# Optimization experiments

Measured on AMD Instinct MI355X. Metric: run time of the kernel, lower is better.

## Reference

```python
import jax, jax.numpy as jnp
import numpy as np

ALPHA = 0.5
EPS = 1e-6


def setup_inputs() -> dict:
    key = jax.random.key(0)
    k1, k2, k3 = jax.random.split(key, 3)
    B, N = 8192, 4096
    y_pred = jax.random.uniform(k1, (B, N), dtype=jnp.float32)
    y_true = jax.random.randint(k2, (B, N), 0, 2).astype(jnp.float32)
    depth_weights = jax.random.uniform(k3, (B, N), dtype=jnp.float32)
    return {"y_pred": y_pred, "y_true": y_true, "depth_weights": depth_weights}


def reference(y_pred, y_true, depth_weights):
    B, N = y_true.shape
    # --- weighted BCE ---
    bce = -(y_true * jnp.log(y_pred + EPS) + (1.0 - y_true) * jnp.log(1.0 - y_pred + EPS))
    wbce = jnp.mean(depth_weights * bce)

    # --- continuity-weighted loss: max run of correct predictions per row ---
    y_bin = (y_pred > 0.5).astype(y_true.dtype)
    correct = (y_bin == y_true)  # bool [B, N]
    idx = jnp.arange(N, dtype=jnp.int32)
    # position (1-based) of most recent incorrect element; 0 if none yet
    reset = jnp.where(correct, 0, idx + 1)  # [B, N]
    last_reset = jax.lax.cummax(reset, axis=1)  # [B, N]
    streak = (idx + 1)[None, :] - last_reset  # current run length at each position
    max_streak = jnp.max(streak, axis=1).astype(jnp.float32)  # [B]
    cwl = jnp.mean(1.0 - max_streak / N)

    return ALPHA * wbce + (1.0 - ALPHA) * cwl
```

## Files before the change

kernel.cpp:

```cpp
#include <hip/hip_runtime.h>

#define EPS 1e-6f
#define LN2F 0.69314718055994530942f


#define ONE(pc, tc, wc, bit) {                                   \
    const bool  tb  = (tc) != 0.0f;   \
    const float sel = tb ? (pc) : 1.0f - (pc);                   \
    sum = fmaf((wc), __log2f(sel + EPS), sum);                   \
    nibs |= (unsigned)(((pc) > 0.5f) == tb) << (bit); }

#define CHUNK(P, T, W, q) {                  \
    ONE(P.x, T.x, W.x, 8*(q)+0)              \
    ONE(P.y, T.y, W.y, 8*(q)+1)              \
    ONE(P.z, T.z, W.z, 8*(q)+2)              \
    ONE(P.w, T.w, W.w, 8*(q)+3) }

__global__ __launch_bounds__(256, 4) void phaseA_kernel(
        const float* __restrict__ yp, const float* __restrict__ yt,
        const float* __restrict__ dw,
        unsigned short* __restrict__ masks,
        float* __restrict__ wv_wbce,
        long tiles_total) {
    const int lane = threadIdx.x & 63;
    const int wave = threadIdx.x >> 6;
    const long wgid = (long)blockIdx.x * 4 + wave;
    const long nwv  = (long)gridDim.x * 4;

    __shared__ unsigned nibbuf[256];

    float sum = 0.0f;

    for (long t = wgid; t < tiles_total; t += nwv) {
        const long base = t * 1024 + lane * 4;
        const float4* pp = (const float4*)(yp + base);
        const float4* tp = (const float4*)(yt + base);
        const float4* wp = (const float4*)(dw + base);

        const float4 p0 = pp[0],   p1 = pp[64],  p2 = pp[128], p3 = pp[192];
        const float4 t0 = tp[0],   t1 = tp[64],  t2 = tp[128], t3 = tp[192];
        const float4 w0 = wp[0],   w1 = wp[64],  w2 = wp[128], w3 = wp[192];

        unsigned nibs = 0;
        CHUNK(p0, t0, w0, 0)
        CHUNK(p1, t1, w1, 1)
        CHUNK(p2, t2, w2, 2)
        CHUNK(p3, t3, w3, 3)

        nibbuf[wave * 64 + lane] = nibs;
        asm volatile("s_waitcnt lgkmcnt(0)" ::: "memory");
        const uint4 d = *(const uint4*)&nibbuf[wave * 64 + 4 * (lane & 15)];
        const int qs = (lane >> 4) * 8;
        const unsigned mask = ((d.x >> qs) & 0xFu)
                            | (((d.y >> qs) & 0xFu) << 4)
                            | (((d.z >> qs) & 0xFu) << 8)
                            | (((d.w >> qs) & 0xFu) << 12);
        masks[t * 64 + (lane >> 4) * 16 + (lane & 15)] = (unsigned short)mask;
    }

    #pragma unroll
    for (int off = 32; off; off >>= 1) sum += __shfl_down(sum, off);
    if (lane == 0) wv_wbce[wgid] = sum;
}

__global__ __launch_bounds__(256, 4) void phaseB_kernel(
        const unsigned short* __restrict__ masks,
        int* __restrict__ wv_streak, long rows) {
    const int lane = threadIdx.x & 63;
    const int wave = threadIdx.x >> 6;
    const long wgid = (long)blockIdx.x * 4 + wave;
    const long nwv  = (long)gridDim.x * 4;

    int acc = 0;
    for (long r = wgid; r < rows; r += nwv) {
        const unsigned long long m =
            *(const unsigned long long*)(masks + r * 256 + lane * 4);
        int pre, suf, mx;
        if (~m == 0ULL) {
            pre = suf = mx = 64;
        } else {
            pre = __builtin_ctzll(~m);
            suf = __builtin_clzll(~m);
            const unsigned long long pp1 = m;
            const unsigned long long pp2 = pp1 & (pp1 << 1);
            const unsigned long long pp4 = pp2 & (pp2 << 2);
            const unsigned long long pp8 = pp4 & (pp4 << 4);
            const unsigned long long pp16 = pp8 & (pp8 << 8);
            const unsigned long long pp32 = pp16 & (pp16 << 16);
            unsigned long long z; int len;
            if (pp32)      { z = pp32; len = 32; }
            else if (pp16) { z = pp16; len = 16; }
            else if (pp8)  { z = pp8;  len = 8; }
            else if (pp4)  { z = pp4;  len = 4; }
            else if (pp2)  { z = pp2;  len = 2; }
            else           { z = pp1;  len = 1; }
            { const unsigned long long q = (z << 16) & pp16; if (q) { z = q; len += 16; } }
            { const unsigned long long q = (z << 8)  & pp8;  if (q) { z = q; len += 8; } }
            { const unsigned long long q = (z << 4)  & pp4;  if (q) { z = q; len += 4; } }
            { const unsigned long long q = (z << 2)  & pp2;  if (q) { z = q; len += 2; } }
            { const unsigned long long q = (z << 1)  & pp1;  if (q) { z = q; len += 1; } }
            mx = m ? len : 0;
        }

        int alen = 64;
        #pragma unroll
        for (int off = 1; off < 64; off <<= 1) {
            const int bpre = __shfl_down(pre, off);
            const int bsuf = __shfl_down(suf, off);
            const int bmx  = __shfl_down(mx,  off);
            const int npre = (pre == alen) ? (alen + bpre) : pre;
            const int nsuf = (bsuf == alen) ? (alen + suf) : bsuf;
            mx  = max(max(mx, bmx), suf + bpre);
            pre = npre; suf = nsuf; alen <<= 1;
        }
        if (lane == 0) acc += mx;
    }
    if (lane == 0) wv_streak[wgid] = acc;
}

__global__ __launch_bounds__(1024) void finalize_kernel(
        const float* __restrict__ wv_wbce, int nA,
        const int* __restrict__ wv_streak, int nB,
        long long total_elems, float* __restrict__ out) {
    double s = 0.0;
    long long st = 0;
    for (int i = threadIdx.x; i < nA; i += 1024) s  += (double)wv_wbce[i];
    for (int i = threadIdx.x; i < nB; i += 1024) st += (long long)wv_streak[i];
    __shared__ double sd[1024];
    __shared__ long long sl[1024];
    sd[threadIdx.x] = s; sl[threadIdx.x] = st;
    __syncthreads();
    for (int o = 512; o; o >>= 1) {
        if (threadIdx.x < o) {
            sd[threadIdx.x] += sd[threadIdx.x + o];
            sl[threadIdx.x] += sl[threadIdx.x + o];
        }
        __syncthreads();
    }
    if (threadIdx.x == 0) {
        const double total = (double)total_elems;
        const double wbce = -LN2F * sd[0] / total;
        const double cwl  = 1.0 - (double)sl[0] / total;
        out[0] = (float)(0.5 * wbce + 0.5 * cwl);
    }
}

struct RunStats { int len, pre, suf, mx; };
__device__ inline RunStats rcombine(const RunStats& a, const RunStats& b) {
    RunStats r;
    r.len = a.len + b.len;
    r.pre = (a.pre == a.len) ? (a.len + b.pre) : a.pre;
    r.suf = (b.suf == b.len) ? (b.len + a.suf) : b.suf;
    r.mx  = max(max(a.mx, b.mx), a.suf + b.pre);
    return r;
}

__global__ __launch_bounds__(256) void fb_row_kernel(
        const float* __restrict__ yp, const float* __restrict__ yt,
        const float* __restrict__ dw,
        float* __restrict__ row_wbce, int* __restrict__ row_streak) {
    const int row  = blockIdx.x;
    const int lane = threadIdx.x & 63;
    const int wave = threadIdx.x >> 6;
    const long base = (long)row * 4096 + wave * 1024 + lane * 4;
    const float4* pp = (const float4*)(yp + base);
    const float4* tp = (const float4*)(yt + base);
    const float4* wp = (const float4*)(dw + base);

    float sum = 0.0f;
    unsigned nibs = 0;
    #pragma unroll
    for (int q = 0; q < 4; ++q) {
        const float4 P = pp[q * 64];
        const float4 T = tp[q * 64];
        const float4 W = wp[q * 64];
        CHUNK(P, T, W, q)
    }
    __shared__ unsigned nibbuf[256];
    nibbuf[wave * 64 + lane] = nibs;
    __syncthreads();
    const uint4 d = *(const uint4*)&nibbuf[wave * 64 + 4 * (lane & 15)];
    const int qs = (lane >> 4) * 8;
    const unsigned mask = ((d.x >> qs) & 0xFu) | (((d.y >> qs) & 0xFu) << 4)
                        | (((d.z >> qs) & 0xFu) << 8) | (((d.w >> qs) & 0xFu) << 12);
    const int pre = __builtin_ctz(~mask);
    const int suf = __builtin_clz(~(mask << 16));
    int mx;
    {
        const unsigned p1 = mask, p2 = p1 & (p1 << 1), p4 = p2 & (p2 << 2), p8 = p4 & (p4 << 4);
        unsigned z; int len;
        if (p8) { z = p8; len = 8; } else if (p4) { z = p4; len = 4; }
        else if (p2) { z = p2; len = 2; } else { z = p1; len = 1; }
        { const unsigned q2 = (z << 8) & p8; if (q2) { z = q2; len += 8; } }
        { const unsigned q2 = (z << 4) & p4; if (q2) { z = q2; len += 4; } }
        { const unsigned q2 = (z << 2) & p2; if (q2) { z = q2; len += 2; } }
        { const unsigned q2 = (z << 1) & p1; if (q2) { z = q2; len += 1; } }
        mx = mask ? len : 0;
    }
    #pragma unroll
    for (int off = 32; off; off >>= 1) sum += __shfl_down(sum, off);
    int packed = pre | (suf << 10) | (mx << 20);
    int alen = 16;
    #pragma unroll
    for (int off = 1; off < 32; off <<= 1) {
        const int o = __shfl_down(packed, off);
        const int apre = packed & 1023, asuf = (packed >> 10) & 1023, amx = packed >> 20;
        const int bpre = o & 1023, bsuf = (o >> 10) & 1023, bmx = o >> 20;
        packed = ((apre == alen) ? (alen + bpre) : apre)
               | (((bsuf == alen) ? (alen + asuf) : bsuf) << 10)
               | (max(max(amx, bmx), asuf + bpre) << 20);
        alen <<= 1;
    }
    RunStats g;
    {
        const int o = __shfl_down(packed, 32);
        const int apre = packed & 1023, asuf = (packed >> 10) & 1023, amx = packed >> 20;
        const int bpre = o & 1023, bsuf = (o >> 10) & 1023, bmx = o >> 20;
        g.len = 1024;
        g.pre = (apre == 512) ? (512 + bpre) : apre;
        g.suf = (bsuf == 512) ? (512 + asuf) : bsuf;
        g.mx  = max(max(amx, bmx), asuf + bpre);
    }
    __shared__ RunStats sstat[4];
    __shared__ float ssum[4];
    if (lane == 0) { sstat[wave] = g; ssum[wave] = sum; }
    __syncthreads();
    if (threadIdx.x == 0) {
        RunStats r = rcombine(rcombine(sstat[0], sstat[1]), rcombine(sstat[2], sstat[3]));
        row_wbce[row]   = -LN2F * (ssum[0] + ssum[1] + ssum[2] + ssum[3]);
        row_streak[row] = r.mx;
    }
}

__global__ __launch_bounds__(1024) void fb_finalize_kernel(
        const float* __restrict__ row_wbce, const int* __restrict__ row_streak,
        int rows, float* __restrict__ out) {
    double s = 0.0; long long st = 0;
    for (int i = threadIdx.x; i < rows; i += 1024) {
        s += (double)row_wbce[i]; st += (long long)row_streak[i];
    }
    __shared__ double sd[1024];
    __shared__ long long sl[1024];
    sd[threadIdx.x] = s; sl[threadIdx.x] = st;
    __syncthreads();
    for (int o = 512; o; o >>= 1) {
        if (threadIdx.x < o) { sd[threadIdx.x] += sd[threadIdx.x + o]; sl[threadIdx.x] += sl[threadIdx.x + o]; }
        __syncthreads();
    }
    if (threadIdx.x == 0) {
        const double total = (double)rows * 4096.0;
        out[0] = (float)(0.5 * (sd[0] / total) + 0.5 * (1.0 - (double)sl[0] / total));
    }
}

extern "C" void kernel_launch(void* const* d_in, const int* in_sizes, int n_in,
                              void* d_out, int out_size, void* d_ws, size_t ws_size,
                              hipStream_t stream) {
    const float* yp = (const float*)d_in[0];
    const float* yt = (const float*)d_in[1];
    const float* dw = (const float*)d_in[2];
    float* out = (float*)d_out;

    const long rows = in_sizes[0] / 4096;
    const long long total = (long long)rows * 4096;

    const size_t mask_bytes = (size_t)rows * 512;
    const size_t off_wbce   = mask_bytes;
    const size_t off_streak = off_wbce + 8192 * sizeof(float);
    const size_t need       = off_streak + 1024 * sizeof(int);

    if (ws_size >= need) {
        unsigned short* masks  = (unsigned short*)d_ws;
        float* wv_wbce         = (float*)((char*)d_ws + off_wbce);
        int*   wv_streak       = (int*)((char*)d_ws + off_streak);
        const long tiles_total = total / 1024;

        phaseA_kernel<<<2048, 256, 0, stream>>>(yp, yt, dw, masks, wv_wbce, tiles_total);
        phaseB_kernel<<<256, 256, 0, stream>>>(masks, wv_streak, rows);
        finalize_kernel<<<1, 1024, 0, stream>>>(wv_wbce, 8192, wv_streak, 1024, total, out);
    } else {
        float* row_wbce   = (float*)d_ws;
        int*   row_streak = (int*)((char*)d_ws + (size_t)rows * sizeof(float));
        fb_row_kernel<<<(int)rows, 256, 0, stream>>>(yp, yt, dw, row_wbce, row_streak);
        fb_finalize_kernel<<<1, 1024, 0, stream>>>(row_wbce, row_streak, (int)rows, out);
    }
}
```

Before: 360.7 us.

## Double-buffer phaseA inputs via async global-to-LDS loads

PhaseA now streams each wave's tile of y_pred, y_true and depth weights into LDS with global_load_lds and double-buffers it, issuing the next tile's loads before computing the current one. Blocks shrink to 128 threads and the grid doubles, so the number of waves stays 8192. The aim is to hide memory latency in a bandwidth-bound reduction. The cost is 48KB of LDS per block, which limits occupancy, plus an extra LDS read pass.

```diff
diff --git a/kernel.cpp b/kernel.cpp
--- a/kernel.cpp
+++ b/kernel.cpp
@@ -3,20 +3,28 @@
 #define EPS 1e-6f
 #define LN2F 0.69314718055994530942f
 
-
-#define ONE(pc, tc, wc, bit) {                                   \
+#define ONEB(pc, tc, wc, bit) {                                  \
     const bool  tb  = (tc) != 0.0f;   \
     const float sel = tb ? (pc) : 1.0f - (pc);                   \
     sum = fmaf((wc), __log2f(sel + EPS), sum);                   \
     nibs |= (unsigned)(((pc) > 0.5f) == tb) << (bit); }
 
-#define CHUNK(P, T, W, q) {                  \
-    ONE(P.x, T.x, W.x, 8*(q)+0)              \
-    ONE(P.y, T.y, W.y, 8*(q)+1)              \
-    ONE(P.z, T.z, W.z, 8*(q)+2)              \
-    ONE(P.w, T.w, W.w, 8*(q)+3) }
-
-__global__ __launch_bounds__(256, 4) void phaseA_kernel(
+#define CHUNK_FB(P, T, W, q) {               \
+    ONEB(P.x, T.x, W.x, 8*(q)+0)             \
+    ONEB(P.y, T.y, W.y, 8*(q)+1)             \
+    ONEB(P.z, T.z, W.z, 8*(q)+2)             \
+    ONEB(P.w, T.w, W.w, 8*(q)+3) }
+
+#define VMWAIT(N) { asm volatile("s_waitcnt vmcnt(" #N ")" ::: "memory"); \
+                    __builtin_amdgcn_sched_barrier(0); }
+
+__device__ __forceinline__ void gload_lds16(const float* g, float* l) {
+    __builtin_amdgcn_global_load_lds(
+        (const __attribute__((address_space(1))) void*)g,
+        (__attribute__((address_space(3)))       void*)l, 16, 0, 0);
+}
+
+__global__ __launch_bounds__(128) void phaseA_kernel(
         const float* __restrict__ yp, const float* __restrict__ yt,
         const float* __restrict__ dw,
         unsigned short* __restrict__ masks,
@@ -24,28 +32,62 @@
         long tiles_total) {
     const int lane = threadIdx.x & 63;
     const int wave = threadIdx.x >> 6;
-    const long wgid = (long)blockIdx.x * 4 + wave;
-    const long nwv  = (long)gridDim.x * 4;
-
-    __shared__ unsigned nibbuf[256];
+    const long wgid = (long)blockIdx.x * 2 + wave;
+    const long nwv  = (long)gridDim.x * 2;
+
+    __shared__ __align__(16) float sbuf[2][2][3][1024];
+    __shared__ unsigned nibbuf[128];
 
     float sum = 0.0f;
 
-    for (long t = wgid; t < tiles_total; t += nwv) {
-        const long base = t * 1024 + lane * 4;
-        const float4* pp = (const float4*)(yp + base);
-        const float4* tp = (const float4*)(yt + base);
-        const float4* wp = (const float4*)(dw + base);
-
-        const float4 p0 = pp[0],   p1 = pp[64],  p2 = pp[128], p3 = pp[192];
-        const float4 t0 = tp[0],   t1 = tp[64],  t2 = tp[128], t3 = tp[192];
-        const float4 w0 = wp[0],   w1 = wp[64],  w2 = wp[128], w3 = wp[192];
+    auto ISSUE = [&](long t, int par) {
+        const float* gp = yp + t * 1024 + lane * 4;
+        const float* gt = yt + t * 1024 + lane * 4;
+        const float* gw = dw + t * 1024 + lane * 4;
+        #pragma unroll
+        for (int c = 0; c < 4; ++c) {
+            gload_lds16(gp + c * 256, &sbuf[wave][par][0][c * 256]);
+            gload_lds16(gt + c * 256, &sbuf[wave][par][1][c * 256]);
+            gload_lds16(gw + c * 256, &sbuf[wave][par][2][c * 256]);
+        }
+    };
+
+    long t  = wgid;
+    int par = 0;
+    if (t < tiles_total) ISSUE(t, 0);
+
+    for (; t < tiles_total; t += nwv, par ^= 1) {
+        const long tn = t + nwv;
+        if (tn < tiles_total) {
+            ISSUE(tn, par ^ 1);
+            VMWAIT(12)
+        } else {
+            VMWAIT(0)
+        }
+
+        const float* pb = &sbuf[wave][par][0][0];
+        const float* tb = &sbuf[wave][par][1][0];
+        const float* wb = &sbuf[wave][par][2][0];
+        const int lo = lane * 4;
+
+        const float4 p0 = *(const float4*)(pb + lo);
+        const float4 p1 = *(const float4*)(pb + lo + 256);
+        const float4 p2 = *(const float4*)(pb + lo + 512);
+        const float4 p3 = *(const float4*)(pb + lo + 768);
+        const float4 t0 = *(const float4*)(tb + lo);
+        const float4 t1 = *(const float4*)(tb + lo + 256);
+        const float4 t2 = *(const float4*)(tb + lo + 512);
+        const float4 t3 = *(const float4*)(tb + lo + 768);
+        const float4 w0 = *(const float4*)(wb + lo);
+        const float4 w1 = *(const float4*)(wb + lo + 256);
+        const float4 w2 = *(const float4*)(wb + lo + 512);
+        const float4 w3 = *(const float4*)(wb + lo + 768);
 
         unsigned nibs = 0;
-        CHUNK(p0, t0, w0, 0)
-        CHUNK(p1, t1, w1, 1)
-        CHUNK(p2, t2, w2, 2)
-        CHUNK(p3, t3, w3, 3)
+        CHUNK_FB(p0, t0, w0, 0)
+        CHUNK_FB(p1, t1, w1, 1)
+        CHUNK_FB(p2, t2, w2, 2)
+        CHUNK_FB(p3, t3, w3, 3)
 
         nibbuf[wave * 64 + lane] = nibs;
         asm volatile("s_waitcnt lgkmcnt(0)" ::: "memory");
@@ -174,7 +216,7 @@
         const float4 P = pp[q * 64];
         const float4 T = tp[q * 64];
         const float4 W = wp[q * 64];
-        CHUNK(P, T, W, q)
+        CHUNK_FB(P, T, W, q)
     }
     __shared__ unsigned nibbuf[256];
     nibbuf[wave * 64 + lane] = nibs;
@@ -270,12 +312,12 @@
     const size_t need       = off_streak + 1024 * sizeof(int);
 
     if (ws_size >= need) {
-        unsigned short* masks  = (unsigned short*)d_ws;
-        float* wv_wbce         = (float*)((char*)d_ws + off_wbce);
-        int*   wv_streak       = (int*)((char*)d_ws + off_streak);
+        unsigned short* masks = (unsigned short*)d_ws;
+        float* wv_wbce   = (float*)((char*)d_ws + off_wbce);
+        int*   wv_streak = (int*)((char*)d_ws + off_streak);
         const long tiles_total = total / 1024;
 
-        phaseA_kernel<<<2048, 256, 0, stream>>>(yp, yt, dw, masks, wv_wbce, tiles_total);
+        phaseA_kernel<<<4096, 128, 0, stream>>>(yp, yt, dw, masks, wv_wbce, tiles_total);
         phaseB_kernel<<<256, 256, 0, stream>>>(masks, wv_streak, rows);
         finalize_kernel<<<1, 1024, 0, stream>>>(wv_wbce, 8192, wv_streak, 1024, total, out);
     } else {
```

After: 361.9 us. About the same (+0.3%).
